# Kernel optimization log

Measured on AMD Instinct MI355X. Metric: run time of the kernel, lower is better.

## Reference

```python
import jax, jax.numpy as jnp
import numpy as np

DIM = 4096
BATCH = 8192
NUM_LAYERS = 6
STRENGTHS = (0.1, 0.1, 0.05)  # entail, contra, neutral
EPS_NORM = 1e-12  # torch F.normalize eps
MAX_NORM = 10.0


def _normalize(x, axis=-1):
    n = jnp.linalg.norm(x, axis=axis, keepdims=True)
    return x / jnp.maximum(n, EPS_NORM)


def setup_inputs() -> dict:
    key = jax.random.key(0)
    k0, k1, k2, k3 = jax.random.split(key, 4)
    return {
        "h0": jax.random.normal(k0, (BATCH, DIM), dtype=jnp.float32),
        "anchor_entail": jax.random.normal(k1, (DIM,), dtype=jnp.float32),
        "anchor_contra": jax.random.normal(k2, (DIM,), dtype=jnp.float32),
        "anchor_neutral": jax.random.normal(k3, (DIM,), dtype=jnp.float32),
    }


def reference(h0, anchor_entail, anchor_contra, anchor_neutral):
    # Normalized fixed anchor directions, stacked [3, dim] (E, C, N)
    dirs = jnp.stack([
        _normalize(anchor_entail, axis=0),
        _normalize(anchor_contra, axis=0),
        _normalize(anchor_neutral, axis=0),
    ])  # [3, dim]
    strengths = jnp.asarray(STRENGTHS, dtype=h0.dtype)  # [3]

    def step(h, _):
        h_n = _normalize(h)                         # [B, dim]
        align = jnp.einsum("bd,kd->bk", h_n, dirs)  # [B, 3]
        div = 1.0 - align                           # divergence_from_alignment
        tens = jnp.maximum(div, 0.0)                # tension (clamp min=0)
        # normalized direction away from each anchor: [B, 3, dim]
        vec = _normalize(h[:, None, :] - dirs[None, :, :])
        force = jnp.einsum("bk,bkd->bd", strengths[None, :] * div, vec)
        h = h - force
        h_norm = jnp.linalg.norm(h, axis=-1, keepdims=True)
        h = jnp.where(h_norm > MAX_NORM, h * (MAX_NORM / (h_norm + 1e-8)), h)
        return h, (align, div, tens)

    h_final, (aligns, divs, tensions) = jax.lax.scan(step, h0, None, length=NUM_LAYERS)
    # traces: [num_layers, B, 3] with anchor order (entail, contra, neutral)
    return h_final, aligns, divs, tensions
```

## Files before the change

### kernel.cpp

```cpp
#include <hip/hip_runtime.h>


constexpr int DIM = 4096;
constexpr int BATCH = 8192;
constexpr int NLAYERS = 6;
constexpr int TPB = 256;
constexpr int VPT = DIM / (TPB * 4);

constexpr size_t HOUT = (size_t)BATCH * DIM;
constexpr size_t TRACE = (size_t)NLAYERS * BATCH * 3;
constexpr size_t OFF_ALIGN = HOUT;
constexpr size_t OFF_DIV   = HOUT + TRACE;
constexpr size_t OFF_TENS  = HOUT + 2 * TRACE;

__device__ __forceinline__ float wave_red(float v) {
#pragma unroll
  for (int off = 32; off > 0; off >>= 1) v += __shfl_down(v, off, 64);
  return v;
}

__global__ __launch_bounds__(TPB) void collapse_kernel(
    const float* __restrict__ h0,
    const float* __restrict__ an0,
    const float* __restrict__ an1,
    const float* __restrict__ an2,
    float* __restrict__ out) {
  const int b = blockIdx.x;
  const int tid = threadIdx.x;
  const float* hrow = h0 + (size_t)b * DIM;

  float4 hv[VPT], a0v[VPT], a1v[VPT], a2v[VPT];
  float r[10];
#pragma unroll
  for (int i = 0; i < 10; ++i) r[i] = 0.f;

#pragma unroll
  for (int j = 0; j < VPT; ++j) {
    const int idx = (tid + j * TPB) * 4;
    hv[j]  = *(const float4*)(hrow + idx);
    a0v[j] = *(const float4*)(an0 + idx);
    a1v[j] = *(const float4*)(an1 + idx);
    a2v[j] = *(const float4*)(an2 + idx);
    const float4 h = hv[j], x = a0v[j], y = a1v[j], z = a2v[j];
    r[0] += h.x*h.x + h.y*h.y + h.z*h.z + h.w*h.w;
    r[1] += h.x*x.x + h.y*x.y + h.z*x.z + h.w*x.w;
    r[2] += h.x*y.x + h.y*y.y + h.z*y.z + h.w*y.w;
    r[3] += h.x*z.x + h.y*z.y + h.z*z.z + h.w*z.w;
    r[4] += x.x*x.x + x.y*x.y + x.z*x.z + x.w*x.w;
    r[5] += y.x*y.x + y.y*y.y + y.z*y.z + y.w*y.w;
    r[6] += z.x*z.x + z.y*z.y + z.z*z.z + z.w*z.w;
    r[7] += x.x*y.x + x.y*y.y + x.z*y.z + x.w*y.w;
    r[8] += x.x*z.x + x.y*z.y + x.z*z.z + x.w*z.w;
    r[9] += y.x*z.x + y.y*z.y + y.z*z.z + y.w*z.w;
  }

  __shared__ float lds[4][10];
  const int lane = tid & 63, wv = tid >> 6;
#pragma unroll
  for (int i = 0; i < 10; ++i) r[i] = wave_red(r[i]);
  if (lane == 0) {
#pragma unroll
    for (int i = 0; i < 10; ++i) lds[wv][i] = r[i];
  }
  __syncthreads();
#pragma unroll
  for (int i = 0; i < 10; ++i)
    r[i] = lds[0][i] + lds[1][i] + lds[2][i] + lds[3][i];

  const float n0 = fmaxf(sqrtf(r[4]), 1e-12f);
  const float n1 = fmaxf(sqrtf(r[5]), 1e-12f);
  const float n2 = fmaxf(sqrtf(r[6]), 1e-12f);
  float G[3][3];
  G[0][0] = r[4] / (n0 * n0);
  G[1][1] = r[5] / (n1 * n1);
  G[2][2] = r[6] / (n2 * n2);
  G[0][1] = G[1][0] = r[7] / (n0 * n1);
  G[0][2] = G[2][0] = r[8] / (n0 * n2);
  G[1][2] = G[2][1] = r[9] / (n1 * n2);

  const float str[3] = {0.1f, 0.1f, 0.05f};
  float s = r[0];
  float d[3] = {r[1] / n0, r[2] / n1, r[3] / n2};
  float A = 1.f;
  float B[3] = {0.f, 0.f, 0.f};

#pragma unroll
  for (int l = 0; l < NLAYERS; ++l) {
    const float hn = fmaxf(sqrtf(s), 1e-12f);
    float al[3], dv[3], c[3];
#pragma unroll
    for (int k = 0; k < 3; ++k) {
      al[k] = d[k] / hn;
      dv[k] = 1.f - al[k];
      const float rr = fmaxf(sqrtf(s - 2.f * d[k] + G[k][k]), 1e-12f);
      c[k] = str[k] * dv[k] / rr;
    }
    if (tid == 0) {
#pragma unroll
      for (int k = 0; k < 3; ++k) {
        const size_t o = (size_t)l * (BATCH * 3) + (size_t)b * 3 + k;
        out[OFF_ALIGN + o] = al[k];
        out[OFF_DIV + o]   = dv[k];
        out[OFF_TENS + o]  = fmaxf(dv[k], 0.f);
      }
    }
    const float a = 1.f - (c[0] + c[1] + c[2]);
    float dn[3];
#pragma unroll
    for (int j = 0; j < 3; ++j)
      dn[j] = a * d[j] + c[0] * G[0][j] + c[1] * G[1][j] + c[2] * G[2][j];
    float sn = a * a * s + 2.f * a * (c[0]*d[0] + c[1]*d[1] + c[2]*d[2]);
#pragma unroll
    for (int k = 0; k < 3; ++k)
#pragma unroll
      for (int j = 0; j < 3; ++j) sn += c[k] * c[j] * G[k][j];
    A = a * A;
#pragma unroll
    for (int j = 0; j < 3; ++j) B[j] = a * B[j] + c[j];
    s = sn;
#pragma unroll
    for (int j = 0; j < 3; ++j) d[j] = dn[j];
    const float hn2 = sqrtf(s);
    if (hn2 > 10.0f) {
      const float sc = 10.0f / (hn2 + 1e-8f);
      A *= sc;
#pragma unroll
      for (int j = 0; j < 3; ++j) { B[j] *= sc; d[j] *= sc; }
      s *= sc * sc;
    }
  }

  const float w0 = B[0] / n0, w1 = B[1] / n1, w2 = B[2] / n2;
  float* orow = out + (size_t)b * DIM;
#pragma unroll
  for (int j = 0; j < VPT; ++j) {
    const int idx = (tid + j * TPB) * 4;
    const float4 h = hv[j], x = a0v[j], y = a1v[j], z = a2v[j];
    float4 o;
    o.x = A * h.x + w0 * x.x + w1 * y.x + w2 * z.x;
    o.y = A * h.y + w0 * x.y + w1 * y.y + w2 * z.y;
    o.z = A * h.z + w0 * x.z + w1 * y.z + w2 * z.z;
    o.w = A * h.w + w0 * x.w + w1 * y.w + w2 * z.w;
    *(float4*)(orow + idx) = o;
  }
}

extern "C" void kernel_launch(void* const* d_in, const int* in_sizes, int n_in,
                              void* d_out, int out_size, void* d_ws, size_t ws_size,
                              hipStream_t stream) {
  const float* h0  = (const float*)d_in[0];
  const float* an0 = (const float*)d_in[1];
  const float* an1 = (const float*)d_in[2];
  const float* an2 = (const float*)d_in[3];
  float* out = (float*)d_out;
  collapse_kernel<<<BATCH, TPB, 0, stream>>>(h0, an0, an1, an2, out);
}
```

Measured before the change: 268.0 us.

## Precompute anchor Gram matrix once and scalar recurrence in one thread

Moves the anchor norms and Gram matrix into a separate single-block pre-kernel that writes them to workspace, so each row block reduces only four dot products instead of ten. The per-layer scalar recurrence now runs on thread 0 and is broadcast through shared memory, and anchor vectors are reloaded from cache in the output pass instead of being held in registers. This cuts reduction work and register pressure, which may allow higher occupancy. The cost is an extra kernel launch, a second barrier, and repeated anchor loads that should hit cache.

```diff
diff --git a/kernel.cpp b/kernel.cpp
--- a/kernel.cpp
+++ b/kernel.cpp
@@ -19,83 +19,118 @@
   return v;
 }
 
+__global__ __launch_bounds__(TPB) void gram_kernel(
+    const float* __restrict__ an0, const float* __restrict__ an1,
+    const float* __restrict__ an2, float* __restrict__ ws) {
+  const int tid = threadIdx.x;
+  float r[6];
+#pragma unroll
+  for (int i = 0; i < 6; ++i) r[i] = 0.f;
+#pragma unroll
+  for (int j = 0; j < VPT; ++j) {
+    const int idx = (tid + j * TPB) * 4;
+    const float4 x = *(const float4*)(an0 + idx);
+    const float4 y = *(const float4*)(an1 + idx);
+    const float4 z = *(const float4*)(an2 + idx);
+    r[0] += x.x*x.x + x.y*x.y + x.z*x.z + x.w*x.w;
+    r[1] += y.x*y.x + y.y*y.y + y.z*y.z + y.w*y.w;
+    r[2] += z.x*z.x + z.y*z.y + z.z*z.z + z.w*z.w;
+    r[3] += x.x*y.x + x.y*y.y + x.z*y.z + x.w*y.w;
+    r[4] += x.x*z.x + x.y*z.y + x.z*z.z + x.w*z.w;
+    r[5] += y.x*z.x + y.y*z.y + y.z*z.z + y.w*z.w;
+  }
+  __shared__ float lds[4][6];
+  const int lane = tid & 63, wv = tid >> 6;
+#pragma unroll
+  for (int i = 0; i < 6; ++i) r[i] = wave_red(r[i]);
+  if (lane == 0) {
+#pragma unroll
+    for (int i = 0; i < 6; ++i) lds[wv][i] = r[i];
+  }
+  __syncthreads();
+  if (tid == 0) {
+#pragma unroll
+    for (int i = 0; i < 6; ++i)
+      r[i] = lds[0][i] + lds[1][i] + lds[2][i] + lds[3][i];
+    const float n0 = fmaxf(sqrtf(r[0]), 1e-12f);
+    const float n1 = fmaxf(sqrtf(r[1]), 1e-12f);
+    const float n2 = fmaxf(sqrtf(r[2]), 1e-12f);
+    ws[0] = n0; ws[1] = n1; ws[2] = n2;
+    ws[3] = r[3] / (n0 * n1);
+    ws[4] = r[4] / (n0 * n2);
+    ws[5] = r[5] / (n1 * n2);
+    ws[6] = r[0] / (n0 * n0);
+    ws[7] = r[1] / (n1 * n1);
+    ws[8] = r[2] / (n2 * n2);
+  }
+}
+
 __global__ __launch_bounds__(TPB) void collapse_kernel(
     const float* __restrict__ h0,
     const float* __restrict__ an0,
     const float* __restrict__ an1,
     const float* __restrict__ an2,
+    const float* __restrict__ ws,
     float* __restrict__ out) {
   const int b = blockIdx.x;
   const int tid = threadIdx.x;
   const float* hrow = h0 + (size_t)b * DIM;
 
-  float4 hv[VPT], a0v[VPT], a1v[VPT], a2v[VPT];
-  float r[10];
-#pragma unroll
-  for (int i = 0; i < 10; ++i) r[i] = 0.f;
-
+  float4 hv[VPT];
+  float r[4] = {0.f, 0.f, 0.f, 0.f};
 #pragma unroll
   for (int j = 0; j < VPT; ++j) {
     const int idx = (tid + j * TPB) * 4;
-    hv[j]  = *(const float4*)(hrow + idx);
-    a0v[j] = *(const float4*)(an0 + idx);
-    a1v[j] = *(const float4*)(an1 + idx);
-    a2v[j] = *(const float4*)(an2 + idx);
-    const float4 h = hv[j], x = a0v[j], y = a1v[j], z = a2v[j];
+    hv[j] = *(const float4*)(hrow + idx);
+    const float4 x = *(const float4*)(an0 + idx);
+    const float4 y = *(const float4*)(an1 + idx);
+    const float4 z = *(const float4*)(an2 + idx);
+    const float4 h = hv[j];
     r[0] += h.x*h.x + h.y*h.y + h.z*h.z + h.w*h.w;
     r[1] += h.x*x.x + h.y*x.y + h.z*x.z + h.w*x.w;
     r[2] += h.x*y.x + h.y*y.y + h.z*y.z + h.w*y.w;
     r[3] += h.x*z.x + h.y*z.y + h.z*z.z + h.w*z.w;
-    r[4] += x.x*x.x + x.y*x.y + x.z*x.z + x.w*x.w;
-    r[5] += y.x*y.x + y.y*y.y + y.z*y.z + y.w*y.w;
-    r[6] += z.x*z.x + z.y*z.y + z.z*z.z + z.w*z.w;
-    r[7] += x.x*y.x + x.y*y.y + x.z*y.z + x.w*y.w;
-    r[8] += x.x*z.x + x.y*z.y + x.z*z.z + x.w*z.w;
-    r[9] += y.x*z.x + y.y*z.y + y.z*z.z + y.w*z.w;
-  }
-
-  __shared__ float lds[4][10];
+  }
+
+  __shared__ float lds[4][4];
+  __shared__ float coef[4];
   const int lane = tid & 63, wv = tid >> 6;
 #pragma unroll
-  for (int i = 0; i < 10; ++i) r[i] = wave_red(r[i]);
+  for (int i = 0; i < 4; ++i) r[i] = wave_red(r[i]);
   if (lane == 0) {
 #pragma unroll
-    for (int i = 0; i < 10; ++i) lds[wv][i] = r[i];
+    for (int i = 0; i < 4; ++i) lds[wv][i] = r[i];
   }
   __syncthreads();
-#pragma unroll
-  for (int i = 0; i < 10; ++i)
-    r[i] = lds[0][i] + lds[1][i] + lds[2][i] + lds[3][i];
-
-  const float n0 = fmaxf(sqrtf(r[4]), 1e-12f);
-  const float n1 = fmaxf(sqrtf(r[5]), 1e-12f);
-  const float n2 = fmaxf(sqrtf(r[6]), 1e-12f);
-  float G[3][3];
-  G[0][0] = r[4] / (n0 * n0);
-  G[1][1] = r[5] / (n1 * n1);
-  G[2][2] = r[6] / (n2 * n2);
-  G[0][1] = G[1][0] = r[7] / (n0 * n1);
-  G[0][2] = G[2][0] = r[8] / (n0 * n2);
-  G[1][2] = G[2][1] = r[9] / (n1 * n2);
-
-  const float str[3] = {0.1f, 0.1f, 0.05f};
-  float s = r[0];
-  float d[3] = {r[1] / n0, r[2] / n1, r[3] / n2};
-  float A = 1.f;
-  float B[3] = {0.f, 0.f, 0.f};
-
-#pragma unroll
-  for (int l = 0; l < NLAYERS; ++l) {
-    const float hn = fmaxf(sqrtf(s), 1e-12f);
-    float al[3], dv[3], c[3];
-#pragma unroll
-    for (int k = 0; k < 3; ++k) {
-      al[k] = d[k] / hn;
-      dv[k] = 1.f - al[k];
-      const float rr = fmaxf(sqrtf(s - 2.f * d[k] + G[k][k]), 1e-12f);
-      c[k] = str[k] * dv[k] / rr;
-    }
-    if (tid == 0) {
+
+  if (tid == 0) {
+#pragma unroll
+    for (int i = 0; i < 4; ++i)
+      r[i] = lds[0][i] + lds[1][i] + lds[2][i] + lds[3][i];
+    const float n0 = ws[0], n1 = ws[1], n2 = ws[2];
+    float G[3][3];
+    G[0][1] = G[1][0] = ws[3];
+    G[0][2] = G[2][0] = ws[4];
+    G[1][2] = G[2][1] = ws[5];
+    G[0][0] = ws[6]; G[1][1] = ws[7]; G[2][2] = ws[8];
+
+    const float str[3] = {0.1f, 0.1f, 0.05f};
+    float s = r[0];
+    float d[3] = {r[1] / n0, r[2] / n1, r[3] / n2};
+    float A = 1.f;
+    float B[3] = {0.f, 0.f, 0.f};
+
+#pragma unroll
+    for (int l = 0; l < NLAYERS; ++l) {
+      const float hn = fmaxf(sqrtf(s), 1e-12f);
+      float al[3], dv[3], c[3];
+#pragma unroll
+      for (int k = 0; k < 3; ++k) {
+        al[k] = d[k] / hn;
+        dv[k] = 1.f - al[k];
+        const float rr = fmaxf(sqrtf(s - 2.f * d[k] + G[k][k]), 1e-12f);
+        c[k] = str[k] * dv[k] / rr;
+      }
 #pragma unroll
       for (int k = 0; k < 3; ++k) {
         const size_t o = (size_t)l * (BATCH * 3) + (size_t)b * 3 + k;
@@ -103,39 +138,47 @@
         out[OFF_DIV + o]   = dv[k];
         out[OFF_TENS + o]  = fmaxf(dv[k], 0.f);
       }
+      const float a = 1.f - (c[0] + c[1] + c[2]);
+      float dn[3];
+#pragma unroll
+      for (int j = 0; j < 3; ++j)
+        dn[j] = a * d[j] + c[0] * G[0][j] + c[1] * G[1][j] + c[2] * G[2][j];
+      float sn = a * a * s + 2.f * a * (c[0]*d[0] + c[1]*d[1] + c[2]*d[2]);
+#pragma unroll
+      for (int k = 0; k < 3; ++k)
+#pragma unroll
+        for (int j = 0; j < 3; ++j) sn += c[k] * c[j] * G[k][j];
+      A = a * A;
+#pragma unroll
+      for (int j = 0; j < 3; ++j) B[j] = a * B[j] + c[j];
+      s = sn;
+#pragma unroll
+      for (int j = 0; j < 3; ++j) d[j] = dn[j];
+      const float hn2 = sqrtf(s);
+      if (hn2 > 10.0f) {
+        const float sc = 10.0f / (hn2 + 1e-8f);
+        A *= sc;
+#pragma unroll
+        for (int j = 0; j < 3; ++j) { B[j] *= sc; d[j] *= sc; }
+        s *= sc * sc;
+      }
     }
-    const float a = 1.f - (c[0] + c[1] + c[2]);
-    float dn[3];
-#pragma unroll
-    for (int j = 0; j < 3; ++j)
-      dn[j] = a * d[j] + c[0] * G[0][j] + c[1] * G[1][j] + c[2] * G[2][j];
-    float sn = a * a * s + 2.f * a * (c[0]*d[0] + c[1]*d[1] + c[2]*d[2]);
-#pragma unroll
-    for (int k = 0; k < 3; ++k)
-#pragma unroll
-      for (int j = 0; j < 3; ++j) sn += c[k] * c[j] * G[k][j];
-    A = a * A;
-#pragma unroll
-    for (int j = 0; j < 3; ++j) B[j] = a * B[j] + c[j];
-    s = sn;
-#pragma unroll
-    for (int j = 0; j < 3; ++j) d[j] = dn[j];
-    const float hn2 = sqrtf(s);
-    if (hn2 > 10.0f) {
-      const float sc = 10.0f / (hn2 + 1e-8f);
-      A *= sc;
-#pragma unroll
-      for (int j = 0; j < 3; ++j) { B[j] *= sc; d[j] *= sc; }
-      s *= sc * sc;
-    }
-  }
-
-  const float w0 = B[0] / n0, w1 = B[1] / n1, w2 = B[2] / n2;
+    coef[0] = A;
+    coef[1] = B[0] / n0;
+    coef[2] = B[1] / n1;
+    coef[3] = B[2] / n2;
+  }
+  __syncthreads();
+  const float A = coef[0], w0 = coef[1], w1 = coef[2], w2 = coef[3];
+
   float* orow = out + (size_t)b * DIM;
 #pragma unroll
   for (int j = 0; j < VPT; ++j) {
     const int idx = (tid + j * TPB) * 4;
-    const float4 h = hv[j], x = a0v[j], y = a1v[j], z = a2v[j];
+    const float4 x = *(const float4*)(an0 + idx);
+    const float4 y = *(const float4*)(an1 + idx);
+    const float4 z = *(const float4*)(an2 + idx);
+    const float4 h = hv[j];
     float4 o;
     o.x = A * h.x + w0 * x.x + w1 * y.x + w2 * z.x;
     o.y = A * h.y + w0 * x.y + w1 * y.y + w2 * z.y;
@@ -153,5 +196,7 @@
   const float* an1 = (const float*)d_in[2];
   const float* an2 = (const float*)d_in[3];
   float* out = (float*)d_out;
-  collapse_kernel<<<BATCH, TPB, 0, stream>>>(h0, an0, an1, an2, out);
-}
+  float* ws  = (float*)d_ws;
+  gram_kernel<<<1, TPB, 0, stream>>>(an0, an1, an2, ws);
+  collapse_kernel<<<BATCH, TPB, 0, stream>>>(h0, an0, an1, an2, ws, out);
+}
```

After: 259.7 us. 3.1% less time.
